# Kernel optimization log

Hardware: AMD Instinct MI355X
Metric: run time of the kernel (lower is better)

## Reference

```python
import jax, jax.numpy as jnp
import numpy as np

B, N, D, E, H = 8, 256, 128, 32, 4
HD = D // H
EPS = 1e-5


def setup_inputs() -> dict:
    key = jax.random.key(0)
    ks = jax.random.split(key, 20)
    idx = jnp.arange(N)

    h = jax.random.normal(ks[0], (B, N, D), dtype=jnp.float32)
    adj = (jax.random.uniform(ks[1], (B, N, N)) < 0.5).astype(jnp.float32)
    adj = adj.at[:, idx, idx].set(1.0)
    edge_features = jax.random.normal(ks[2], (B, N, N, E), dtype=jnp.float32)
    src_mask = (jax.random.uniform(ks[3], (B, N, N)) < 0.7).astype(jnp.float32)
    src_mask = src_mask.at[:, idx, idx].set(1.0)

    s = 1.0 / np.sqrt(D)
    se = 1.0 / np.sqrt(E)
    p = {
        "gcn_w": jax.random.normal(ks[4], (D, D)) * s,
        "gcn_b": jnp.zeros((D,)),
        "edge_w": jax.random.normal(ks[5], (D, E)) * se,
        "edge_b": jnp.zeros((D,)),
        "wq": jax.random.normal(ks[6], (D, D)) * s,
        "wk": jax.random.normal(ks[7], (D, D)) * s,
        "wv": jax.random.normal(ks[8], (D, D)) * s,
        "bq": jnp.zeros((D,)),
        "bk": jnp.zeros((D,)),
        "bv": jnp.zeros((D,)),
        "out_w": jax.random.normal(ks[9], (D, D)) * s,
        "out_b": jnp.zeros((D,)),
        "ln_g": jnp.ones((D,)),
        "ln_b": jnp.zeros((D,)),
    }
    return {"h": h, "adj": adj, "edge_features": edge_features, "src_mask": src_mask, **p}


def reference(h, adj, edge_features, src_mask,
              gcn_w, gcn_b, edge_w, edge_b,
              wq, wk, wv, bq, bk, bv, out_w, out_b, ln_g, ln_b):
    b, n, d = h.shape

    # --- GCN branch: degree-normalized aggregation with self-loops ---
    adj_sl = adj + jnp.eye(n, dtype=h.dtype)[None]          # (B,N,N)
    deg = adj_sl.sum(-1, keepdims=True)                      # (B,N,1)
    h_agg = jnp.einsum('bnm,bmd->bnd', adj_sl, h) / deg
    h_gcn = h_agg @ gcn_w.T + gcn_b                          # (B,N,D)

    # --- edge-conditioned key/value: h_ij = h_j + edge_emb ---
    edge_emb = jnp.einsum('bnme,de->bnmd', edge_features, edge_w) + edge_b
    h_ij = h[:, None, :, :] + edge_emb                       # (B,N,N,D)

    # key padding mask: True where edge absent (masked)
    masked = (adj * src_mask) == 0                           # (B,N,N)

    # --- multi-head attention, one query per node ---
    q = (h @ wq.T + bq).reshape(b, n, H, HD)                 # (B,N,H,HD)
    k = (jnp.einsum('bnmd,ed->bnme', h_ij, wk) + bk).reshape(b, n, n, H, HD)
    v = (jnp.einsum('bnmd,ed->bnme', h_ij, wv) + bv).reshape(b, n, n, H, HD)

    scores = jnp.einsum('bnhd,bnmhd->bnhm', q, k) / np.sqrt(HD)  # (B,N,H,N)
    scores = jnp.where(masked[:, :, None, :], -jnp.inf, scores)
    attn = jax.nn.softmax(scores, axis=-1)
    o = jnp.einsum('bnhm,bnmhd->bnhd', attn, v).reshape(b, n, d)
    o = o @ out_w.T + out_b                                  # (B,N,D)

    # residual + layernorm (dropout is identity in eval)
    x = h + o
    mu = x.mean(-1, keepdims=True)
    var = ((x - mu) ** 2).mean(-1, keepdims=True)
    h_attn = ln_g * (x - mu) / jnp.sqrt(var + EPS) + ln_b

    return h_gcn + h_attn
```

## Files before the change

kernel.cpp:

```cpp
#include <hip/hip_runtime.h>
#include <hip/hip_bf16.h>

#define OFF_WQT 0
#define OFF_WKT 16384
#define OFF_WVT 32768
#define OFF_OWT 49152
#define OFF_GWT 65536
#define OFF_WKE 81920
#define OFF_WVET 86016
#define OFF_KB  90112
#define OFF_VB  90240
#define OFF_SC  90368
#define OFF_QSP 98560
#define OFF_QEP 229632
#define OFF_HG  360704
#define OFF_K0P 622848
#define OFF_V0P 753920

using half2_t = __attribute__((ext_vector_type(2))) __fp16;

static __device__ __forceinline__ half2_t u2h(unsigned int u){
  union { unsigned int u; half2_t h; } x; x.u = u; return x.h;
}
static __device__ __forceinline__ unsigned int pkf16(float a, float b){
  union { half2_t h; unsigned int u; } x;
  x.h = __builtin_amdgcn_cvt_pkrtz(a, b);
  return x.u;
}
static __device__ __forceinline__ float fdot2(unsigned int a, unsigned int b, float c){
  return __builtin_amdgcn_fdot2(u2h(a), u2h(b), c, false);
}

__global__ __launch_bounds__(256) void prep_kernel(
    const float* __restrict__ wq, const float* __restrict__ wk,
    const float* __restrict__ wv, const float* __restrict__ out_w,
    const float* __restrict__ gcn_w, const float* __restrict__ edge_w,
    const float* __restrict__ edge_b, const float* __restrict__ bk,
    const float* __restrict__ bv, float* __restrict__ ws)
{
  int blk = blockIdx.x, t = threadIdx.x;
  if (blk < 320) {
    int w = blk >> 6;
    int e0 = (blk & 63) * 256 + t;
    const float* src = (w==0) ? wq : (w==1) ? wk : (w==2) ? wv : (w==3) ? out_w : gcn_w;
    float* dst = ws + ((w==0) ? OFF_WQT : (w==1) ? OFF_WKT : (w==2) ? OFF_WVT
                      : (w==3) ? OFF_OWT : OFF_GWT);
    int k = e0 >> 7, d = e0 & 127;
    dst[e0] = src[d*128 + k];
  } else if (blk < 352) {
    int idx = blk - 320;
    int which = idx >> 4;
    int e0 = (idx & 15) * 256 + t;
    int dd = e0 >> 5, e = e0 & 31;
    const float* W = which ? wv : wk;
    float acc = 0.f;
    #pragma unroll 4
    for (int k2 = 0; k2 < 128; ++k2) acc += W[dd*128+k2] * edge_w[k2*32+e];
    if (which) ws[OFF_WVET + e*128 + dd] = acc;
    else       ws[OFF_WKE + e0] = acc;
  } else {
    int dd = t & 127;
    const float* W  = (t < 128) ? wk : wv;
    const float* bb = (t < 128) ? bk : bv;
    float acc = bb[dd];
    #pragma unroll 4
    for (int k2 = 0; k2 < 128; ++k2) acc += W[dd*128+k2] * edge_b[k2];
    ws[((t < 128) ? OFF_KB : OFF_VB) + dd] = acc;
  }
}

__global__ __launch_bounds__(256) void proj_kernel(
    const float* __restrict__ h, const float* __restrict__ adj,
    const float* __restrict__ bq, const float* __restrict__ gcn_b,
    float* __restrict__ ws)
{
  __shared__ float h_lds[256];
  __shared__ float adj_lds[512];
  __shared__ float p1[2][2][128];
  __shared__ float p2[2][2][128];
  __shared__ float p3[2][2][128];
  __shared__ float qrow[2*132];
  __shared__ float qe_l[2*132];
  __shared__ float dpart[2][2];
  __shared__ float ha_lds[2*132];

  int t = threadIdx.x;
  int d = t & 127, kh = t >> 7;
  int r0 = blockIdx.x * 2;
  int b  = r0 >> 8, n0 = r0 & 255;
  unsigned int* wsu = (unsigned int*)ws;

  if (t < 64)  ((float4*)h_lds)[t]   = ((const float4*)(h   + (size_t)r0*128))[t];
  if (t < 128) ((float4*)adj_lds)[t] = ((const float4*)(adj + (size_t)r0*256))[t];
  __syncthreads();

  {
    const float* wqT = ws + OFF_WQT;
    const float* wkT = ws + OFF_WKT;
    const float* wvT = ws + OFF_WVT;
    float aq0=0,aq1=0,ak0=0,ak1=0,av0=0,av1=0;
    #pragma unroll 4
    for (int kk = 0; kk < 64; ++kk) {
      int k = kh*64 + kk;
      float qw = wqT[k*128+d], kw = wkT[k*128+d], vw = wvT[k*128+d];
      float h0 = h_lds[k], h1 = h_lds[128+k];
      aq0 += qw*h0; aq1 += qw*h1;
      ak0 += kw*h0; ak1 += kw*h1;
      av0 += vw*h0; av1 += vw*h1;
    }
    p1[kh][0][d]=aq0; p1[kh][1][d]=aq1;
    p2[kh][0][d]=ak0; p2[kh][1][d]=ak1;
    p3[kh][0][d]=av0; p3[kh][1][d]=av1;
  }
  __syncthreads();

  {
    int i = t >> 7, dd = t & 127;
    const float inv = 0.17677669529663687f;
    qrow[i*132 + dd] = (p1[0][i][dd] + p1[1][i][dd] + bq[dd]) * inv;
  }
  {
    int i = (t >> 6) & 1, pr = t & 63;
    if (t < 128) {
      float k0 = p2[0][i][2*pr] + p2[1][i][2*pr];
      float k1 = p2[0][i][2*pr+1] + p2[1][i][2*pr+1];
      wsu[OFF_K0P + (size_t)(r0+i)*64 + pr] = pkf16(k0, k1);
    } else {
      float v0 = p3[0][i][2*pr] + p3[1][i][2*pr];
      float v1 = p3[0][i][2*pr+1] + p3[1][i][2*pr+1];
      wsu[OFF_V0P + (size_t)(r0+i)*64 + pr] = pkf16(v0, v1);
    }
  }
  __syncthreads();

  if (t < 128) {
    int i = t >> 6, pr = t & 63;
    wsu[OFF_QSP + (size_t)(r0+i)*64 + pr] = pkf16(qrow[i*132 + 2*pr], qrow[i*132 + 2*pr+1]);
  }
  {
    int i = t >> 7, he = t & 127, hh = he >> 5, e = he & 31;
    float acc = 0.f;
    #pragma unroll
    for (int j = 0; j < 32; ++j)
      acc += ws[OFF_WKE + (hh*32 + j)*32 + e] * qrow[i*132 + hh*32 + j];
    qe_l[i*132 + he] = acc;
  }
  if (t < 8) {
    int i = t >> 2, hh = t & 3;
    float acc = 0.f;
    #pragma unroll
    for (int j = 0; j < 32; ++j)
      acc += qrow[i*132 + hh*32 + j] * ws[OFF_KB + hh*32 + j];
    ws[OFF_SC + (size_t)(r0+i)*4 + hh] = acc;
  }
  {
    float ag0=0, ag1=0, dg0=0, dg1=0;
    #pragma unroll 4
    for (int mm = 0; mm < 128; ++mm) {
      int ml = kh*128 + mm;
      float hv = h[((size_t)b*256 + ml)*128 + d];
      float a0 = adj_lds[ml]       + ((ml == n0)     ? 1.0f : 0.0f);
      float a1 = adj_lds[256 + ml] + ((ml == n0 + 1) ? 1.0f : 0.0f);
      ag0 += a0*hv; ag1 += a1*hv; dg0 += a0; dg1 += a1;
    }
    p1[kh][0][d]=ag0; p1[kh][1][d]=ag1;
    if (d == 0) { dpart[kh][0]=dg0; dpart[kh][1]=dg1; }
  }
  __syncthreads();

  if (t < 128) {
    int i = t >> 6, pr = t & 63;
    wsu[OFF_QEP + (size_t)(r0+i)*64 + pr] = pkf16(qe_l[i*132 + 2*pr], qe_l[i*132 + 2*pr+1]);
  }
  {
    int i = t >> 7, dd = t & 127;
    ha_lds[i*132 + dd] = (p1[0][i][dd] + p1[1][i][dd]) / (dpart[0][i] + dpart[1][i]);
  }
  __syncthreads();

  {
    const float* gwT = ws + OFF_GWT;
    float g0=0, g1=0;
    #pragma unroll 4
    for (int kk = 0; kk < 64; ++kk) {
      int k = kh*64 + kk;
      float gw = gwT[k*128+d];
      g0 += gw * ha_lds[k];
      g1 += gw * ha_lds[132 + k];
    }
    p2[kh][0][d]=g0; p2[kh][1][d]=g1;
  }
  __syncthreads();
  {
    int i = t >> 7, dd = t & 127;
    ws[OFF_HG + (size_t)(r0+i)*128 + dd] = p2[0][i][dd] + p2[1][i][dd] + gcn_b[dd];
  }
}

__global__ __launch_bounds__(256, 5) void attn_kernel(
    const float* __restrict__ edge, const float* __restrict__ adj,
    const float* __restrict__ srcm, const float* __restrict__ h,
    const float* __restrict__ out_b, const float* __restrict__ ln_g,
    const float* __restrict__ ln_b, const float* __restrict__ ws,
    float* __restrict__ out)
{
  __shared__ unsigned int e_lds[256*18];
  __shared__ float s_buf[4*264];
  __shared__ float part4[4*132];
  __shared__ float part5[4*132];
  __shared__ float wpart[16];

  float* const s_lds = s_buf;
  float* const eb_l  = s_buf;
  float* const o_l   = s_buf + 132;
  float* const px    = s_buf + 264;
  float* const stat  = s_buf + 520;

  const int t  = threadIdx.x;
  const int bn = blockIdx.x;
  const int b  = bn >> 8;
  const int hh = t & 3;
  const int mq = t >> 2;
  const unsigned int* wsu = (const unsigned int*)ws;

  const float4* et = (const float4*)(edge + (size_t)bn*8192);

  float4 va = et[t];
  float4 vb = et[256 + t];
  float mp_my = adj[(size_t)bn*256 + t] * srcm[(size_t)bn*256 + t];

  unsigned int qs_pk[16], qe_pk[16];
  {
    const uint4* qp = (const uint4*)(wsu + OFF_QSP + (size_t)bn*64 + hh*16);
    const uint4* qe = (const uint4*)(wsu + OFF_QEP + (size_t)bn*64 + hh*16);
    #pragma unroll
    for (int j = 0; j < 4; ++j) {
      uint4 a = qp[j];
      qs_pk[4*j+0]=a.x; qs_pk[4*j+1]=a.y; qs_pk[4*j+2]=a.z; qs_pk[4*j+3]=a.w;
      uint4 c = qe[j];
      qe_pk[4*j+0]=c.x; qe_pk[4*j+1]=c.y; qe_pk[4*j+2]=c.z; qe_pk[4*j+3]=c.w;
    }
  }
  float sconst = ws[OFF_SC + (size_t)bn*4 + hh];
  const unsigned int* K0 = wsu + OFF_K0P + (size_t)b*256*64;

  float exacc = 0.f;
  #pragma unroll
  for (int c = 0; c < 4; ++c) {
    {
      int fi = c*512 + t;
      int row = fi >> 3, c4 = fi & 7;
      uint2 pk;
      pk.x = pkf16(va.x, va.y);
      pk.y = pkf16(va.z, va.w);
      *(uint2*)(e_lds + row*18 + c4*2) = pk;
      int fj = fi + 256;
      int row2 = fj >> 3, c42 = fj & 7;
      uint2 pk2;
      pk2.x = pkf16(vb.x, vb.y);
      pk2.y = pkf16(vb.z, vb.w);
      *(uint2*)(e_lds + row2*18 + c42*2) = pk2;
    }
    if (c == 0) e_lds[t*18 + 16] = __float_as_uint(mp_my);
    if (c < 3) {
      va = et[(c+1)*512 + t];
      vb = et[(c+1)*512 + 256 + t];
    }
    __syncthreads();

    int mm = (c << 6) | mq;
    float acc = sconst;
    __builtin_amdgcn_s_setprio(1);
    const uint4* kr4 = (const uint4*)(K0 + (size_t)mm*64 + hh*16);
    #pragma unroll
    for (int j4 = 0; j4 < 4; ++j4) {
      uint4 kw = kr4[j4];
      acc = fdot2(qs_pk[4*j4+0], kw.x, acc);
      acc = fdot2(qs_pk[4*j4+1], kw.y, acc);
      acc = fdot2(qs_pk[4*j4+2], kw.z, acc);
      acc = fdot2(qs_pk[4*j4+3], kw.w, acc);
    }
    const uint2* er = (const uint2*)(e_lds + mm*18);
    #pragma unroll
    for (int j2 = 0; j2 < 8; ++j2) {
      uint2 w = er[j2];
      acc = fdot2(qe_pk[2*j2+0], w.x, acc);
      acc = fdot2(qe_pk[2*j2+1], w.y, acc);
    }
    __builtin_amdgcn_s_setprio(0);
    float mp = __uint_as_float(e_lds[mm*18 + 16]);
    float ex = (mp == 0.0f) ? 0.0f : __expf(acc);
    s_lds[hh*264 + mm] = ex;
    exacc += ex;
  }
  exacc += __shfl_down(exacc, 4);
  exacc += __shfl_down(exacc, 8);
  exacc += __shfl_down(exacc, 16);
  exacc += __shfl_down(exacc, 32);
  if ((t & 63) < 4) wpart[(t >> 6)*4 + hh] = exacc;
  __syncthreads();

  {
    int w   = t >> 6;
    int ms  = t >> 5;
    int hh4 = (t >> 3) & 3, e4 = t & 7;
    int c   = t & 31,  hh5 = c >> 3;
    float p4x=0,p4y=0,p4z=0,p4w=0;
    float p5x=0,p5y=0,p5z=0,p5w=0;
    const unsigned int* vrow = wsu + OFF_V0P + (size_t)b*256*64;
    __builtin_amdgcn_s_setprio(1);
    for (int jm = 0; jm < 32; ++jm) {
      int mm = ms*32 + jm;
      float a4 = s_lds[hh4*264 + mm];
      uint2 wv2 = *(const uint2*)(e_lds + mm*18 + e4*2);
      half2_t e0 = u2h(wv2.x), e1 = u2h(wv2.y);
      p4x += a4*(float)e0.x; p4y += a4*(float)e0.y;
      p4z += a4*(float)e1.x; p4w += a4*(float)e1.y;
      float a5 = s_lds[hh5*264 + mm];
      uint2 vv = *(const uint2*)(vrow + (size_t)mm*64 + c*2);
      half2_t v0 = u2h(vv.x), v1 = u2h(vv.y);
      p5x += a5*(float)v0.x; p5y += a5*(float)v0.y;
      p5z += a5*(float)v1.x; p5w += a5*(float)v1.y;
    }
    __builtin_amdgcn_s_setprio(0);
    p4x += __shfl_xor(p4x, 32); p4y += __shfl_xor(p4y, 32);
    p4z += __shfl_xor(p4z, 32); p4w += __shfl_xor(p4w, 32);
    p5x += __shfl_xor(p5x, 32); p5y += __shfl_xor(p5y, 32);
    p5z += __shfl_xor(p5z, 32); p5w += __shfl_xor(p5w, 32);
    if ((t & 32) == 0) {
      float4 f4; f4.x=p4x; f4.y=p4y; f4.z=p4z; f4.w=p4w;
      *(float4*)(part4 + w*132 + hh4*32 + e4*4) = f4;
      float4 f5; f5.x=p5x; f5.y=p5y; f5.z=p5z; f5.w=p5w;
      *(float4*)(part5 + w*132 + c*4) = f5;
    }
  }
  __syncthreads();

  float ov_reg = 0.f;
  if (t < 128) {
    int ht = t >> 5;
    float inv = 1.0f / (wpart[ht] + wpart[4+ht] + wpart[8+ht] + wpart[12+ht]);
    float se = 0.f, s2 = 0.f;
    #pragma unroll
    for (int g = 0; g < 4; ++g) { se += part4[g*132 + t]; s2 += part5[g*132 + t]; }
    eb_l[t] = se * inv;
    ov_reg  = s2 * inv;
  }
  __syncthreads();

  if (t < 128) {
    int hd = t >> 5;
    float acc = ov_reg + ws[OFF_VB + t];
    const float* wveT = ws + OFF_WVET;
    #pragma unroll 4
    for (int e = 0; e < 32; ++e) acc += wveT[e*128 + t] * eb_l[hd*32 + e];
    o_l[t] = acc;
  }
  __syncthreads();

  {
    int d = t & 127, kh = t >> 7;
    const float* owT = ws + OFF_OWT;
    float xa = 0.f;
    #pragma unroll 4
    for (int kk = 0; kk < 64; ++kk) {
      int k = kh*64 + kk;
      xa += owT[k*128 + d] * o_l[k];
    }
    px[kh*128 + d] = xa;
  }
  __syncthreads();

  float x = 0.f;
  if (t < 128) {
    x = px[t] + px[128 + t] + out_b[t] + h[(size_t)bn*128 + t];
    float s = x, ss = x*x;
    #pragma unroll
    for (int off = 32; off > 0; off >>= 1) {
      s  += __shfl_down(s,  off);
      ss += __shfl_down(ss, off);
    }
    if ((t & 63) == 0) { stat[t >> 6] = s; stat[2 + (t >> 6)] = ss; }
  }
  __syncthreads();

  if (t < 128) {
    float mu   = (stat[0] + stat[1]) * (1.0f/128.0f);
    float var  = (stat[2] + stat[3]) * (1.0f/128.0f) - mu*mu;
    float rstd = rsqrtf(var + 1e-5f);
    out[(size_t)bn*128 + t] =
        ln_g[t]*(x - mu)*rstd + ln_b[t] + ws[OFF_HG + (size_t)bn*128 + t];
  }
}

extern "C" void kernel_launch(void* const* d_in, const int* in_sizes, int n_in,
                              void* d_out, int out_size, void* d_ws, size_t ws_size,
                              hipStream_t stream) {
  (void)in_sizes; (void)n_in; (void)out_size; (void)ws_size;
  const float* h     = (const float*)d_in[0];
  const float* adj   = (const float*)d_in[1];
  const float* edge  = (const float*)d_in[2];
  const float* srcm  = (const float*)d_in[3];
  const float* gcn_w = (const float*)d_in[4];
  const float* gcn_b = (const float*)d_in[5];
  const float* edge_w= (const float*)d_in[6];
  const float* edge_b= (const float*)d_in[7];
  const float* wq    = (const float*)d_in[8];
  const float* wk    = (const float*)d_in[9];
  const float* wv    = (const float*)d_in[10];
  const float* bq    = (const float*)d_in[11];
  const float* bk    = (const float*)d_in[12];
  const float* bv    = (const float*)d_in[13];
  const float* out_w = (const float*)d_in[14];
  const float* out_b = (const float*)d_in[15];
  const float* ln_g  = (const float*)d_in[16];
  const float* ln_b  = (const float*)d_in[17];

  float* ws  = (float*)d_ws;
  float* out = (float*)d_out;

  prep_kernel<<<353, 256, 0, stream>>>(wq, wk, wv, out_w, gcn_w, edge_w, edge_b, bk, bv, ws);
  proj_kernel<<<1024, 256, 0, stream>>>(h, adj, bq, gcn_b, ws);
  attn_kernel<<<2048, 256, 0, stream>>>(edge, adj, srcm, h, out_b, ln_g, ln_b, ws, out);
}
```

Measured before the change: 186.8 us.

## Precompute q·K0 score matrix in separate kernel, read it in attention

Adds a qk_kernel that computes the node-only part of the attention scores (q·K0) for four query rows per block, sharing each loaded K row across those four queries, and writes a B×H×N×N fp32 score buffer to workspace. The attention kernel then reads one precomputed score per (n,m,h) instead of loading 16 packed K words and doing 16 dot2 ops, and drops its qs register array and the setprio hints. The cost is an extra kernel launch and a 8 MB write-then-read round trip through global memory.

Result: no change. 190.1 us (+1.7%).

```diff
diff --git a/kernel.cpp b/kernel.cpp
--- a/kernel.cpp
+++ b/kernel.cpp
@@ -16,6 +16,7 @@
 #define OFF_HG  360704
 #define OFF_K0P 622848
 #define OFF_V0P 753920
+#define OFF_S0  884992
 
 using half2_t = __attribute__((ext_vector_type(2))) __fp16;
 
@@ -197,6 +198,45 @@
   }
 }
 
+__global__ __launch_bounds__(256) void qk_kernel(float* __restrict__ ws)
+{
+  __shared__ unsigned int q_l[64];
+  const int t   = threadIdx.x;
+  const int blk = blockIdx.x;
+  const int b   = blk >> 8;
+  const int hh  = (blk >> 6) & 3;
+  const int n0  = (blk & 63) * 4;
+  const unsigned int* wsu = (const unsigned int*)ws;
+
+  if (t < 64) {
+    int r = t >> 4, j = t & 15;
+    q_l[t] = wsu[OFF_QSP + ((size_t)b*256 + n0 + r)*64 + hh*16 + j];
+  }
+  __syncthreads();
+
+  const uint4* kp = (const uint4*)(wsu + OFF_K0P + ((size_t)b*256 + t)*64 + hh*16);
+  uint4 k0 = kp[0], k1 = kp[1], k2 = kp[2], k3 = kp[3];
+  float a0=0.f, a1=0.f, a2=0.f, a3=0.f;
+  #pragma unroll
+  for (int g = 0; g < 4; ++g) {
+    uint4 kg = (g==0) ? k0 : (g==1) ? k1 : (g==2) ? k2 : k3;
+    #pragma unroll
+    for (int jj = 0; jj < 4; ++jj) {
+      unsigned int kj = (jj==0) ? kg.x : (jj==1) ? kg.y : (jj==2) ? kg.z : kg.w;
+      int j = g*4 + jj;
+      a0 = fdot2(q_l[j],      kj, a0);
+      a1 = fdot2(q_l[16 + j], kj, a1);
+      a2 = fdot2(q_l[32 + j], kj, a2);
+      a3 = fdot2(q_l[48 + j], kj, a3);
+    }
+  }
+  float* S0 = ws + OFF_S0 + (((size_t)b*4 + hh)*256 + n0)*256;
+  S0[t]       = a0;
+  S0[256 + t] = a1;
+  S0[512 + t] = a2;
+  S0[768 + t] = a3;
+}
+
 __global__ __launch_bounds__(256, 5) void attn_kernel(
     const float* __restrict__ edge, const float* __restrict__ adj,
     const float* __restrict__ srcm, const float* __restrict__ h,
@@ -219,6 +259,7 @@
   const int t  = threadIdx.x;
   const int bn = blockIdx.x;
   const int b  = bn >> 8;
+  const int n  = bn & 255;
   const int hh = t & 3;
   const int mq = t >> 2;
   const unsigned int* wsu = (const unsigned int*)ws;
@@ -229,20 +270,17 @@
   float4 vb = et[256 + t];
   float mp_my = adj[(size_t)bn*256 + t] * srcm[(size_t)bn*256 + t];
 
-  unsigned int qs_pk[16], qe_pk[16];
-  {
-    const uint4* qp = (const uint4*)(wsu + OFF_QSP + (size_t)bn*64 + hh*16);
+  unsigned int qe_pk[16];
+  {
     const uint4* qe = (const uint4*)(wsu + OFF_QEP + (size_t)bn*64 + hh*16);
     #pragma unroll
     for (int j = 0; j < 4; ++j) {
-      uint4 a = qp[j];
-      qs_pk[4*j+0]=a.x; qs_pk[4*j+1]=a.y; qs_pk[4*j+2]=a.z; qs_pk[4*j+3]=a.w;
       uint4 c = qe[j];
       qe_pk[4*j+0]=c.x; qe_pk[4*j+1]=c.y; qe_pk[4*j+2]=c.z; qe_pk[4*j+3]=c.w;
     }
   }
   float sconst = ws[OFF_SC + (size_t)bn*4 + hh];
-  const unsigned int* K0 = wsu + OFF_K0P + (size_t)b*256*64;
+  const float* S0row = ws + OFF_S0 + (((size_t)b*4 + hh)*256 + n)*256;
 
   float exacc = 0.f;
   #pragma unroll
@@ -269,17 +307,7 @@
     __syncthreads();
 
     int mm = (c << 6) | mq;
-    float acc = sconst;
-    __builtin_amdgcn_s_setprio(1);
-    const uint4* kr4 = (const uint4*)(K0 + (size_t)mm*64 + hh*16);
-    #pragma unroll
-    for (int j4 = 0; j4 < 4; ++j4) {
-      uint4 kw = kr4[j4];
-      acc = fdot2(qs_pk[4*j4+0], kw.x, acc);
-      acc = fdot2(qs_pk[4*j4+1], kw.y, acc);
-      acc = fdot2(qs_pk[4*j4+2], kw.z, acc);
-      acc = fdot2(qs_pk[4*j4+3], kw.w, acc);
-    }
+    float acc = sconst + S0row[mm];
     const uint2* er = (const uint2*)(e_lds + mm*18);
     #pragma unroll
     for (int j2 = 0; j2 < 8; ++j2) {
@@ -287,7 +315,6 @@
       acc = fdot2(qe_pk[2*j2+0], w.x, acc);
       acc = fdot2(qe_pk[2*j2+1], w.y, acc);
     }
-    __builtin_amdgcn_s_setprio(0);
     float mp = __uint_as_float(e_lds[mm*18 + 16]);
     float ex = (mp == 0.0f) ? 0.0f : __expf(acc);
     s_lds[hh*264 + mm] = ex;
@@ -308,7 +335,6 @@
     float p4x=0,p4y=0,p4z=0,p4w=0;
     float p5x=0,p5y=0,p5z=0,p5w=0;
     const unsigned int* vrow = wsu + OFF_V0P + (size_t)b*256*64;
-    __builtin_amdgcn_s_setprio(1);
     for (int jm = 0; jm < 32; ++jm) {
       int mm = ms*32 + jm;
       float a4 = s_lds[hh4*264 + mm];
@@ -322,7 +348,6 @@
       p5x += a5*(float)v0.x; p5y += a5*(float)v0.y;
       p5z += a5*(float)v1.x; p5w += a5*(float)v1.y;
     }
-    __builtin_amdgcn_s_setprio(0);
     p4x += __shfl_xor(p4x, 32); p4y += __shfl_xor(p4y, 32);
     p4z += __shfl_xor(p4z, 32); p4w += __shfl_xor(p4w, 32);
     p5x += __shfl_xor(p5x, 32); p5y += __shfl_xor(p5y, 32);
@@ -421,5 +446,6 @@
 
   prep_kernel<<<353, 256, 0, stream>>>(wq, wk, wv, out_w, gcn_w, edge_w, edge_b, bk, bv, ws);
   proj_kernel<<<1024, 256, 0, stream>>>(h, adj, bq, gcn_b, ws);
+  qk_kernel<<<2048, 256, 0, stream>>>(ws);
   attn_kernel<<<2048, 256, 0, stream>>>(edge, adj, srcm, h, out_b, ln_g, ln_b, ws, out);
 }
```
